# Kernel tuning notes

Hardware: AMD Instinct MI355X
Metric: run time of the kernel (lower is better)

The kernel has to match this reference:

```python
import jax, jax.numpy as jnp
import numpy as np

T, B, H = 2048, 32, 512

def setup_inputs() -> dict:
    key = jax.random.key(0)
    k1, k2, k3, k4 = jax.random.split(key, 4)
    hidden = jax.random.normal(k1, (1, B, H), dtype=jnp.float32)
    encoder_outputs = jax.random.normal(k2, (T, B, H), dtype=jnp.float32)
    # nn.Linear(2H, H): weight (H, 2H), bias (H,)
    bound = 1.0 / np.sqrt(2 * H)
    W_attn = jax.random.uniform(k3, (H, 2 * H), dtype=jnp.float32, minval=-bound, maxval=bound)
    b_attn = jax.random.uniform(jax.random.fold_in(k3, 1), (H,), dtype=jnp.float32, minval=-bound, maxval=bound)
    stdv = 1.0 / np.sqrt(H)
    v = jax.random.normal(k4, (H,), dtype=jnp.float32) * stdv
    return {"hidden": hidden, "encoder_outputs": encoder_outputs,
            "W_attn": W_attn, "b_attn": b_attn, "v": v}

def reference(hidden, encoder_outputs, W_attn, b_attn, v):
    # hidden: (1,B,H) -> broadcast to (B,T,H); enc: (T,B,H) -> (B,T,H)
    enc = jnp.transpose(encoder_outputs, (1, 0, 2))          # (B,T,H)
    h = jnp.broadcast_to(hidden[0][:, None, :], enc.shape)   # (B,T,H)
    cat = jnp.concatenate([h, enc], axis=2)                  # (B,T,2H)
    energy = jnp.tanh(jnp.einsum('bth,oh->bto', cat, W_attn) + b_attn)  # (B,T,H)
    scores = jnp.einsum('bth,h->bt', energy, v)              # (B,T)
    return jax.nn.softmax(scores, axis=1)[:, None, :]        # (B,1,T)
```

## Files before the change

kernel.cpp:

```cpp
#include <hip/hip_runtime.h>
#include <hip/hip_bf16.h>


#define TT 2048
#define BB 32
#define HH 512

typedef __attribute__((ext_vector_type(8))) short bf16x8;
typedef __attribute__((ext_vector_type(4))) float f32x4;

static __device__ __forceinline__ unsigned cvt2(float a, float b) {
    union { __hip_bfloat162 h; unsigned u; } cv;
    cv.h = __float22bfloat162_rn(make_float2(a, b));
    return cv.u;
}

static __device__ __forceinline__ unsigned short f2bf(float f) {
    unsigned int u = __float_as_uint(f);
    unsigned int r = (u + 0x7FFFu + ((u >> 16) & 1u)) >> 16;
    return (unsigned short)r;
}

static __device__ __forceinline__ float fast_tanh(float x) {
    float e = __expf(2.0f * x);
    return 1.0f - 2.0f * __builtin_amdgcn_rcpf(1.0f + e);
}

static __device__ __forceinline__ void gload_lds16(const void* g, void* l) {
    __builtin_amdgcn_global_load_lds(
        (const __attribute__((address_space(1))) unsigned int*)g,
        (__attribute__((address_space(3))) unsigned int*)l, 16, 0, 0);
}

__global__ void pack_w2_kernel(const float* __restrict__ W, short* __restrict__ W2p) {
    int idx = blockIdx.x * 256 + threadIdx.x;
    int nt = idx >> 16;
    int ks = (idx >> 13) & 7;
    int s  = idx & 8191;
    int j  = s >> 6;
    int c  = s & 63;
    int kk = c ^ ((j & 7) << 3);
    int o  = nt * 128 + j;
    int k  = ks * 64 + kk;
    W2p[idx] = (short)f2bf(W[o * 1024 + 512 + k]);
}

__global__ void hb_kernel(const float* __restrict__ hidden, const float* __restrict__ W,
                          const float* __restrict__ b_attn, float* __restrict__ hb) {
    __shared__ float hrow[512];
    int b = blockIdx.x >> 1;
    int o = ((blockIdx.x & 1) << 8) + threadIdx.x;
    for (int h = threadIdx.x; h < 512; h += 256) hrow[h] = hidden[b * 512 + h];
    __syncthreads();
    const float4* wr = reinterpret_cast<const float4*>(W + (size_t)o * 1024);
    const float4* hr = reinterpret_cast<const float4*>(hrow);
    float acc = b_attn[o];
#pragma unroll 8
    for (int i = 0; i < 128; ++i) {
        float4 w = wr[i], h4 = hr[i];
        acc += w.x * h4.x + w.y * h4.y + w.z * h4.z + w.w * h4.w;
    }
    hb[b * 512 + o] = acc;
}

__global__ __launch_bounds__(256, 2) void attn_main_kernel(
    const float* __restrict__ enc, const short* __restrict__ W2p,
    const float* __restrict__ hb, const float* __restrict__ v,
    float* __restrict__ scores_part)
{
    __shared__ short As[2][128 * 64];
    __shared__ short Bs[2][128 * 64];
    __shared__ float s_red[2][128];

    const int tid = threadIdx.x;
    const int bid = blockIdx.x;
    const int w = (bid & 7) * 256 + (bid >> 3);
    const int nt = w & 3;
    const int mtile = w >> 2;
    const int b = mtile >> 4;
    const int t0 = (mtile & 15) * 128;

    const int wave = tid >> 6;
    const int lane = tid & 63;
    const int wr = wave >> 1;
    const int wc = wave & 1;
    const int lcol = lane & 15;
    const int lq = lane >> 4;

    const int arow = tid >> 3;
    const int afc = (tid & 7) * 8;
    const float* encbase = enc + ((size_t)(t0 + arow) * BB + b) * HH + afc;
    const short* bsrc = W2p + nt * 65536 + (wave * 4) * 512 + lane * 8;

    f32x4 acc[4][4];
#pragma unroll
    for (int mt = 0; mt < 4; ++mt)
#pragma unroll
        for (int ns = 0; ns < 4; ++ns) acc[mt][ns] = (f32x4){0.f, 0.f, 0.f, 0.f};

    float4 rA0[8], rA1[8];

#define A_LOAD(RA, KS)                                                              \
    {                                                                               \
        _Pragma("unroll")                                                           \
        for (int p = 0; p < 4; ++p) {                                               \
            const float* src = encbase + (size_t)p * 32 * BB * HH + (KS) * 64;      \
            RA[p * 2]     = *reinterpret_cast<const float4*>(src);                  \
            RA[p * 2 + 1] = *reinterpret_cast<const float4*>(src + 4);              \
        }                                                                           \
    }

#define B_STAGE(KS, BUF)                                                            \
    {                                                                               \
        const short* s0 = bsrc + (KS) * 8192;                                       \
        _Pragma("unroll")                                                           \
        for (int c = 0; c < 4; ++c)                                                 \
            gload_lds16(s0 + c * 512, &Bs[BUF][(wave * 4 + c) * 512]);              \
    }

#define A_WRITE(RA, BUF)                                                            \
    {                                                                               \
        _Pragma("unroll")                                                           \
        for (int p = 0; p < 4; ++p) {                                               \
            const int r = p * 32 + arow;                                            \
            uint4 pk;                                                               \
            pk.x = cvt2(RA[p * 2].x, RA[p * 2].y);                                  \
            pk.y = cvt2(RA[p * 2].z, RA[p * 2].w);                                  \
            pk.z = cvt2(RA[p * 2 + 1].x, RA[p * 2 + 1].y);                          \
            pk.w = cvt2(RA[p * 2 + 1].z, RA[p * 2 + 1].w);                          \
            const int cs = afc ^ ((r & 7) << 3);                                    \
            *reinterpret_cast<uint4*>(&As[BUF][r * 64 + cs]) = pk;                  \
        }                                                                           \
    }

#define COMPUTE(BUF)                                                                \
    {                                                                               \
        _Pragma("unroll")                                                           \
        for (int ksub = 0; ksub < 2; ++ksub) {                                      \
            const int kk = ksub * 32 + lq * 8;                                      \
            bf16x8 af[4], bfr[4];                                                   \
            _Pragma("unroll")                                                       \
            for (int mt = 0; mt < 4; ++mt) {                                        \
                const int r = wr * 64 + mt * 16 + lcol;                             \
                af[mt] = *reinterpret_cast<const bf16x8*>(                          \
                    &As[BUF][r * 64 + (kk ^ ((r & 7) << 3))]);                      \
            }                                                                       \
            _Pragma("unroll")                                                       \
            for (int ns = 0; ns < 4; ++ns) {                                        \
                const int j = wc * 64 + ns * 16 + lcol;                             \
                bfr[ns] = *reinterpret_cast<const bf16x8*>(                         \
                    &Bs[BUF][j * 64 + (kk ^ ((j & 7) << 3))]);                      \
            }                                                                       \
            _Pragma("unroll")                                                       \
            for (int mt = 0; mt < 4; ++mt)                                          \
                _Pragma("unroll")                                                   \
                for (int ns = 0; ns < 4; ++ns)                                      \
                    acc[mt][ns] = __builtin_amdgcn_mfma_f32_16x16x32_bf16(          \
                        af[mt], bfr[ns], acc[mt][ns], 0, 0, 0);                     \
        }                                                                           \
    }

    A_LOAD(rA0, 0);
    B_STAGE(0, 0);
    A_WRITE(rA0, 0);
    A_LOAD(rA1, 1);
    __syncthreads();

#pragma unroll
    for (int s2 = 0; s2 < 4; ++s2) {
        const int s = s2 * 2;
        if (s + 2 < 8) A_LOAD(rA0, s + 2);
        B_STAGE(s + 1, 1);
        COMPUTE(0);
        A_WRITE(rA1, 1);
        __syncthreads();
        if (s + 3 < 8) A_LOAD(rA1, s + 3);
        if (s + 2 < 8) B_STAGE(s + 2, 0);
        COMPUTE(1);
        if (s + 2 < 8) {
            A_WRITE(rA0, 0);
            __syncthreads();
        }
    }

    float part[4][4];
#pragma unroll
    for (int mt = 0; mt < 4; ++mt)
#pragma unroll
        for (int j = 0; j < 4; ++j) part[mt][j] = 0.0f;

#pragma unroll
    for (int ns = 0; ns < 4; ++ns) {
        const int o = nt * 128 + wc * 64 + ns * 16 + lcol;
        const float hbv = hb[b * 512 + o];
        const float vv = v[o];
#pragma unroll
        for (int mt = 0; mt < 4; ++mt)
#pragma unroll
            for (int j = 0; j < 4; ++j)
                part[mt][j] = fmaf(fast_tanh(acc[mt][ns][j] + hbv), vv, part[mt][j]);
    }

#pragma unroll
    for (int off = 1; off < 16; off <<= 1)
#pragma unroll
        for (int mt = 0; mt < 4; ++mt)
#pragma unroll
            for (int j = 0; j < 4; ++j)
                part[mt][j] += __shfl_xor(part[mt][j], off, 64);

    if (lcol == 0) {
#pragma unroll
        for (int mt = 0; mt < 4; ++mt)
#pragma unroll
            for (int j = 0; j < 4; ++j)
                s_red[wc][wr * 64 + mt * 16 + lq * 4 + j] = part[mt][j];
    }
    __syncthreads();

    if (tid < 128)
        scores_part[((size_t)nt * BB + b) * TT + t0 + tid] =
            s_red[0][tid] + s_red[1][tid];
}

__global__ void softmax_kernel(const float* __restrict__ sp, float* __restrict__ out) {
    __shared__ float wred[4];
    __shared__ float wsum[4];
    const int b = blockIdx.x;
    const int tid = threadIdx.x;
    float vals[8];
    float mx = -1e30f;
#pragma unroll
    for (int i = 0; i < 8; ++i) {
        const int t = i * 256 + tid;
        const float s = sp[(size_t)b * TT + t] + sp[((size_t)BB + b) * TT + t] +
                        sp[((size_t)2 * BB + b) * TT + t] + sp[((size_t)3 * BB + b) * TT + t];
        vals[i] = s;
        mx = fmaxf(mx, s);
    }
#pragma unroll
    for (int off = 32; off; off >>= 1) mx = fmaxf(mx, __shfl_xor(mx, off, 64));
    if ((tid & 63) == 0) wred[tid >> 6] = mx;
    __syncthreads();
    mx = fmaxf(fmaxf(wred[0], wred[1]), fmaxf(wred[2], wred[3]));
    float s = 0.0f;
#pragma unroll
    for (int i = 0; i < 8; ++i) {
        vals[i] = __expf(vals[i] - mx);
        s += vals[i];
    }
#pragma unroll
    for (int off = 32; off; off >>= 1) s += __shfl_xor(s, off, 64);
    if ((tid & 63) == 0) wsum[tid >> 6] = s;
    __syncthreads();
    s = wsum[0] + wsum[1] + wsum[2] + wsum[3];
    const float inv = 1.0f / s;
#pragma unroll
    for (int i = 0; i < 8; ++i) out[b * TT + i * 256 + tid] = vals[i] * inv;
}

extern "C" void kernel_launch(void* const* d_in, const int* in_sizes, int n_in,
                              void* d_out, int out_size, void* d_ws, size_t ws_size,
                              hipStream_t stream) {
    const float* hidden = (const float*)d_in[0];
    const float* enc    = (const float*)d_in[1];
    const float* W      = (const float*)d_in[2];
    const float* b_attn = (const float*)d_in[3];
    const float* v      = (const float*)d_in[4];
    float* out = (float*)d_out;

    char* base = (char*)d_ws;
    short* W2p = (short*)base;
    float* hb  = (float*)(base + 524288);
    float* sp  = (float*)(base + 524288 + 65536);

    pack_w2_kernel<<<1024, 256, 0, stream>>>(W, W2p);
    hb_kernel<<<64, 256, 0, stream>>>(hidden, W, b_attn, hb);
    attn_main_kernel<<<2048, 256, 0, stream>>>(enc, W2p, hb, v, sp);
    softmax_kernel<<<32, 256, 0, stream>>>(sp, out);
}
```

Measured before the change: 83.49 us.

## Double threads per block in attention GEMM, halving per-wave row tile

Runs the main attention kernel with 512 threads (8 waves) instead of 256. Each wave now computes 32x64 instead of 64x64 of the same 128x128 block tile, and the A/B global-to-LDS loading is redistributed over twice as many threads. This halves accumulator and staging registers per thread to increase wave-level parallelism and latency hiding. In exchange, each wave gets less MFMA reuse per LDS fragment load, and block-wide barriers cover more waves.

```diff
diff --git a/kernel.cpp b/kernel.cpp
--- a/kernel.cpp
+++ b/kernel.cpp
@@ -63,7 +63,7 @@
     hb[b * 512 + o] = acc;
 }
 
-__global__ __launch_bounds__(256, 2) void attn_main_kernel(
+__global__ __launch_bounds__(512, 2) void attn_main_kernel(
     const float* __restrict__ enc, const short* __restrict__ W2p,
     const float* __restrict__ hb, const float* __restrict__ v,
     float* __restrict__ scores_part)
@@ -87,50 +87,45 @@
     const int lcol = lane & 15;
     const int lq = lane >> 4;
 
-    const int arow = tid >> 3;
-    const int afc = (tid & 7) * 8;
+    const int arow = tid >> 2;
+    const int afc = (tid & 3) * 16;
     const float* encbase = enc + ((size_t)(t0 + arow) * BB + b) * HH + afc;
-    const short* bsrc = W2p + nt * 65536 + (wave * 4) * 512 + lane * 8;
-
-    f32x4 acc[4][4];
-#pragma unroll
-    for (int mt = 0; mt < 4; ++mt)
+    const short* bsrc = W2p + nt * 65536 + (size_t)tid * 8;
+
+    f32x4 acc[2][4];
+#pragma unroll
+    for (int mt = 0; mt < 2; ++mt)
 #pragma unroll
         for (int ns = 0; ns < 4; ++ns) acc[mt][ns] = (f32x4){0.f, 0.f, 0.f, 0.f};
 
-    float4 rA0[8], rA1[8];
+    float4 rA0[4], rA1[4];
 
 #define A_LOAD(RA, KS)                                                              \
     {                                                                               \
-        _Pragma("unroll")                                                           \
-        for (int p = 0; p < 4; ++p) {                                               \
-            const float* src = encbase + (size_t)p * 32 * BB * HH + (KS) * 64;      \
-            RA[p * 2]     = *reinterpret_cast<const float4*>(src);                  \
-            RA[p * 2 + 1] = *reinterpret_cast<const float4*>(src + 4);              \
-        }                                                                           \
+        const float* src = encbase + (KS) * 64;                                     \
+        RA[0] = *reinterpret_cast<const float4*>(src);                              \
+        RA[1] = *reinterpret_cast<const float4*>(src + 4);                          \
+        RA[2] = *reinterpret_cast<const float4*>(src + 8);                          \
+        RA[3] = *reinterpret_cast<const float4*>(src + 12);                         \
     }
 
 #define B_STAGE(KS, BUF)                                                            \
     {                                                                               \
         const short* s0 = bsrc + (KS) * 8192;                                       \
-        _Pragma("unroll")                                                           \
-        for (int c = 0; c < 4; ++c)                                                 \
-            gload_lds16(s0 + c * 512, &Bs[BUF][(wave * 4 + c) * 512]);              \
+        gload_lds16(s0,        &Bs[BUF][wave * 512]);                               \
+        gload_lds16(s0 + 4096, &Bs[BUF][4096 + wave * 512]);                        \
     }
 
 #define A_WRITE(RA, BUF)                                                            \
     {                                                                               \
-        _Pragma("unroll")                                                           \
-        for (int p = 0; p < 4; ++p) {                                               \
-            const int r = p * 32 + arow;                                            \
-            uint4 pk;                                                               \
-            pk.x = cvt2(RA[p * 2].x, RA[p * 2].y);                                  \
-            pk.y = cvt2(RA[p * 2].z, RA[p * 2].w);                                  \
-            pk.z = cvt2(RA[p * 2 + 1].x, RA[p * 2 + 1].y);                          \
-            pk.w = cvt2(RA[p * 2 + 1].z, RA[p * 2 + 1].w);                          \
-            const int cs = afc ^ ((r & 7) << 3);                                    \
-            *reinterpret_cast<uint4*>(&As[BUF][r * 64 + cs]) = pk;                  \
-        }                                                                           \
+        uint4 q0, q1;                                                               \
+        q0.x = cvt2(RA[0].x, RA[0].y);  q0.y = cvt2(RA[0].z, RA[0].w);              \
+        q0.z = cvt2(RA[1].x, RA[1].y);  q0.w = cvt2(RA[1].z, RA[1].w);              \
+        q1.x = cvt2(RA[2].x, RA[2].y);  q1.y = cvt2(RA[2].z, RA[2].w);              \
+        q1.z = cvt2(RA[3].x, RA[3].y);  q1.w = cvt2(RA[3].z, RA[3].w);              \
+        const int sw = (arow & 7) << 3;                                             \
+        *reinterpret_cast<uint4*>(&As[BUF][arow * 64 + (afc ^ sw)]) = q0;           \
+        *reinterpret_cast<uint4*>(&As[BUF][arow * 64 + ((afc + 8) ^ sw)]) = q1;     \
     }
 
 #define COMPUTE(BUF)                                                                \
@@ -138,10 +133,10 @@
         _Pragma("unroll")                                                           \
         for (int ksub = 0; ksub < 2; ++ksub) {                                      \
             const int kk = ksub * 32 + lq * 8;                                      \
-            bf16x8 af[4], bfr[4];                                                   \
+            bf16x8 af[2], bfr[4];                                                   \
             _Pragma("unroll")                                                       \
-            for (int mt = 0; mt < 4; ++mt) {                                        \
-                const int r = wr * 64 + mt * 16 + lcol;                             \
+            for (int mt = 0; mt < 2; ++mt) {                                        \
+                const int r = wr * 32 + mt * 16 + lcol;                             \
                 af[mt] = *reinterpret_cast<const bf16x8*>(                          \
                     &As[BUF][r * 64 + (kk ^ ((r & 7) << 3))]);                      \
             }                                                                       \
@@ -152,7 +147,7 @@
                     &Bs[BUF][j * 64 + (kk ^ ((j & 7) << 3))]);                      \
             }                                                                       \
             _Pragma("unroll")                                                       \
-            for (int mt = 0; mt < 4; ++mt)                                          \
+            for (int mt = 0; mt < 2; ++mt)                                          \
                 _Pragma("unroll")                                                   \
                 for (int ns = 0; ns < 4; ++ns)                                      \
                     acc[mt][ns] = __builtin_amdgcn_mfma_f32_16x16x32_bf16(          \
@@ -161,9 +156,9 @@
     }
 
     A_LOAD(rA0, 0);
+    A_LOAD(rA1, 1);
     B_STAGE(0, 0);
     A_WRITE(rA0, 0);
-    A_LOAD(rA1, 1);
     __syncthreads();
 
 #pragma unroll
@@ -183,9 +178,9 @@
         }
     }
 
-    float part[4][4];
-#pragma unroll
-    for (int mt = 0; mt < 4; ++mt)
+    float part[2][4];
+#pragma unroll
+    for (int mt = 0; mt < 2; ++mt)
 #pragma unroll
         for (int j = 0; j < 4; ++j) part[mt][j] = 0.0f;
 
@@ -195,7 +190,7 @@
         const float hbv = hb[b * 512 + o];
         const float vv = v[o];
 #pragma unroll
-        for (int mt = 0; mt < 4; ++mt)
+        for (int mt = 0; mt < 2; ++mt)
 #pragma unroll
             for (int j = 0; j < 4; ++j)
                 part[mt][j] = fmaf(fast_tanh(acc[mt][ns][j] + hbv), vv, part[mt][j]);
@@ -204,17 +199,17 @@
 #pragma unroll
     for (int off = 1; off < 16; off <<= 1)
 #pragma unroll
-        for (int mt = 0; mt < 4; ++mt)
+        for (int mt = 0; mt < 2; ++mt)
 #pragma unroll
             for (int j = 0; j < 4; ++j)
                 part[mt][j] += __shfl_xor(part[mt][j], off, 64);
 
     if (lcol == 0) {
 #pragma unroll
-        for (int mt = 0; mt < 4; ++mt)
+        for (int mt = 0; mt < 2; ++mt)
 #pragma unroll
             for (int j = 0; j < 4; ++j)
-                s_red[wc][wr * 64 + mt * 16 + lq * 4 + j] = part[mt][j];
+                s_red[wc][wr * 32 + mt * 16 + lq * 4 + j] = part[mt][j];
     }
     __syncthreads();
 
@@ -276,6 +271,6 @@
 
     pack_w2_kernel<<<1024, 256, 0, stream>>>(W, W2p);
     hb_kernel<<<64, 256, 0, stream>>>(hidden, W, b_attn, hb);
-    attn_main_kernel<<<2048, 256, 0, stream>>>(enc, W2p, hb, v, sp);
+    attn_main_kernel<<<2048, 512, 0, stream>>>(enc, W2p, hb, v, sp);
     softmax_kernel<<<32, 256, 0, stream>>>(sp, out);
 }
```

Result: slower. 89.57 us (+7.3%).
